# Kernel tuning notes

Measured on AMD Instinct MI355X. Metric: run time of the kernel, lower is better.

The kernel has to match this reference:

```python
import jax, jax.numpy as jnp
import numpy as np

B, K, IN, CH, M, N = 1024, 64, 128, 256, 4, 16


def setup_inputs() -> dict:
    key = jax.random.key(0)
    ks = jax.random.split(key, 12)
    s = 0.02
    return {
        "user_node": jax.random.normal(ks[0], (B, K, IN), jnp.float32),
        "RIS_node": jax.random.normal(ks[1], (B, IN), jnp.float32),
        "cas_channel": jax.random.normal(ks[2], (B, K, 2 * M * N), jnp.float32),
        "d_link": jax.random.normal(ks[3], (B, K, 2 * M), jnp.float32),
        # f2_user: Linear(3*IN -> CH), ReLU, Linear(CH -> CH)
        "W1": jax.random.normal(ks[4], (3 * IN, CH), jnp.float32) * s,
        "b1": jnp.zeros((CH,), jnp.float32),
        "W2": jax.random.normal(ks[5], (CH, CH), jnp.float32) * s,
        "b2": jnp.zeros((CH,), jnp.float32),
        # f3_RIS: Linear(2*IN -> CH), ReLU, Linear(CH -> CH)
        "W3": jax.random.normal(ks[6], (2 * IN, CH), jnp.float32) * s,
        "b3": jnp.zeros((CH,), jnp.float32),
        "W4": jax.random.normal(ks[7], (CH, CH), jnp.float32) * s,
        "b4": jnp.zeros((CH,), jnp.float32),
    }


def _leave_one_out_max(x):
    # x: (B, K, D). Exact leave-one-out max via prefix/suffix cummax, O(K).
    prefix = jax.lax.cummax(x, axis=1)                      # max over 0..k
    suffix = jax.lax.cummax(x[:, ::-1], axis=1)[:, ::-1]    # max over k..K-1
    neg = jnp.full_like(x[:, :1], -jnp.inf)
    left = jnp.concatenate([neg, prefix[:, :-1]], axis=1)   # max over 0..k-1
    right = jnp.concatenate([suffix[:, 1:], neg], axis=1)   # max over k+1..K-1
    return jnp.maximum(left, right)


def reference(user_node, RIS_node, cas_channel, d_link,
              W1, b1, W2, b2, W3, b3, W4, b4):
    b, k, d = user_node.shape
    mean_user = jnp.mean(user_node, axis=1)                 # (B, IN)
    loo_max = _leave_one_out_max(user_node)                 # (B, K, IN)
    ris_b = jnp.broadcast_to(RIS_node[:, None, :], (b, k, d))
    feat = jnp.concatenate([user_node, loo_max, ris_b], axis=-1)  # (B, K, 3*IN)
    h_user = jax.nn.relu(feat @ W1 + b1) @ W2 + b2          # (B, K, CH)
    user_node_update = jnp.concatenate([user_node, h_user], axis=-1)  # (B,K,IN+CH)
    rfeat = jnp.concatenate([RIS_node, mean_user], axis=-1)  # (B, 2*IN)
    h_ris = jax.nn.relu(rfeat @ W3 + b3) @ W4 + b4          # (B, CH)
    RIS_node_update = jnp.concatenate([RIS_node, h_ris], axis=-1)    # (B, IN+CH)
    return user_node_update, RIS_node_update
```

## Files before the change

kernel.cpp:

```cpp
#include <hip/hip_runtime.h>

typedef __attribute__((ext_vector_type(8))) short short8;
typedef __attribute__((ext_vector_type(4))) float f32x4;
typedef __attribute__((ext_vector_type(4))) int i32x4;

__device__ __forceinline__ unsigned short f2bf(float f) {
  unsigned u = __builtin_bit_cast(unsigned, f);
  u += 0x7fffu + ((u >> 16) & 1u);
  return (unsigned short)(u >> 16);
}

__global__ __launch_bounds__(256) void prep(
    const float* __restrict__ user, const float* __restrict__ ris,
    const float* __restrict__ W1, const float* __restrict__ W2,
    const float* __restrict__ W3, const float* __restrict__ W4,
    unsigned short* __restrict__ m1b, unsigned short* __restrict__ m2b,
    int* __restrict__ am, unsigned short* __restrict__ meanb,
    unsigned short* __restrict__ risb,
    unsigned short* __restrict__ W1f, unsigned short* __restrict__ W2f,
    unsigned short* __restrict__ W3f, unsigned short* __restrict__ W4f,
    float* __restrict__ out0, float* __restrict__ out1) {
  if (blockIdx.x < 512) {
    int idx = blockIdx.x * 256 + threadIdx.x;
    int b = idx >> 7, i = idx & 127;
    const float* up = user + (size_t)(b * 64) * 128 + i;
    float* op = out0 + (size_t)(b * 64) * 384 + i;
    float s = 0.f, m1 = -3.402823466e38f, m2 = -3.402823466e38f;
    int amx = 0;
    #pragma unroll 8
    for (int k = 0; k < 64; ++k) {
      float u = up[(size_t)k * 128];
      op[(size_t)k * 384] = u;
      s += u;
      if (u > m1) { m2 = m1; m1 = u; amx = k; }
      else if (u > m2) { m2 = u; }
    }
    m1b[idx] = f2bf(m1);
    m2b[idx] = f2bf(m2);
    am[idx] = amx;
    meanb[idx] = f2bf(s * (1.f / 64.f));
    float rv = ris[idx];
    out1[(size_t)b * 384 + i] = rv;
    risb[idx] = f2bf(rv);
  } else {
    int idx = (blockIdx.x - 512) * 256 + threadIdx.x;
    const float* src; unsigned short* dst; int kb; int rel;
    if (idx < 98304)        { src = W1; dst = W1f; kb = 12; rel = idx; }
    else if (idx < 163840)  { src = W2; dst = W2f; kb = 8;  rel = idx - 98304; }
    else if (idx < 229376)  { src = W3; dst = W3f; kb = 8;  rel = idx - 163840; }
    else                    { src = W4; dst = W4f; kb = 8;  rel = idx - 229376; }
    int kk = rel >> 8, n = rel & 255;
    int lane = (n & 15) | (((kk >> 3) & 3) << 4);
    int di = (((n >> 4) * kb + (kk >> 5)) * 64 + lane) * 8 + (kk & 7);
    dst[di] = f2bf(src[rel]);
  }
}

template<int MODE>
__device__ __forceinline__ void mlp_body(
    int bx, unsigned short* __restrict__ Hb,
    const float* __restrict__ user,
    const unsigned short* __restrict__ m1b, const unsigned short* __restrict__ m2b,
    const int* __restrict__ am,
    const unsigned short* __restrict__ risb, const unsigned short* __restrict__ meanb,
    const unsigned short* __restrict__ Wa, const unsigned short* __restrict__ Wb,
    const float* __restrict__ ba, const float* __restrict__ bb,
    float* __restrict__ out) {
  constexpr int NFS = (MODE == 0) ? 12 : 8;

  const int tid = threadIdx.x;
  const int lane = tid & 63, wn = tid >> 6;
  const int row0 = bx * 64;
  const int r = lane & 15;
  const int k8 = (lane >> 4) * 8;

  f32x4 acc[4][4];
  #pragma unroll
  for (int a = 0; a < 4; ++a)
    #pragma unroll
    for (int q = 0; q < 4; ++q) acc[a][q] = (f32x4)0.f;

  #pragma unroll
  for (int fs = 0; fs < NFS; ++fs) {
    short8 af[4];
    if constexpr (MODE == 0) {
      if (fs < 4) {
        #pragma unroll
        for (int mf = 0; mf < 4; ++mf) {
          const float* p = &user[(size_t)(row0 + mf * 16 + r) * 128 + fs * 32 + k8];
          f32x4 t0 = *(const f32x4*)p;
          f32x4 t1 = *(const f32x4*)(p + 4);
          short8 t;
          #pragma unroll
          for (int j = 0; j < 4; ++j) { t[j] = (short)f2bf(t0[j]); t[4 + j] = (short)f2bf(t1[j]); }
          af[mf] = t;
        }
      } else if (fs < 8) {
        int c0 = bx * 128 + (fs - 4) * 32 + k8;
        short8 m1v = *(const short8*)&m1b[c0];
        short8 m2v = *(const short8*)&m2b[c0];
        i32x4 a0 = *(const i32x4*)&am[c0];
        i32x4 a1 = *(const i32x4*)&am[c0 + 4];
        #pragma unroll
        for (int mf = 0; mf < 4; ++mf) {
          int rr = mf * 16 + r;
          short8 t;
          #pragma unroll
          for (int j = 0; j < 4; ++j) {
            t[j]     = (a0[j] == rr) ? m2v[j]     : m1v[j];
            t[4 + j] = (a1[j] == rr) ? m2v[4 + j] : m1v[4 + j];
          }
          af[mf] = t;
        }
      } else {
        short8 v = *(const short8*)&risb[bx * 128 + (fs - 8) * 32 + k8];
        #pragma unroll
        for (int mf = 0; mf < 4; ++mf) af[mf] = v;
      }
    } else {
      const unsigned short* src = (fs < 4) ? risb : meanb;
      #pragma unroll
      for (int mf = 0; mf < 4; ++mf)
        af[mf] = *(const short8*)&src[(size_t)(row0 + mf * 16 + r) * 128 + (fs & 3) * 32 + k8];
    }
    short8 bfr[4];
    #pragma unroll
    for (int nf = 0; nf < 4; ++nf)
      bfr[nf] = *(const short8*)&Wa[(size_t)(((wn * 4 + nf) * NFS + fs) * 64 + lane) * 8];
    #pragma unroll
    for (int mf = 0; mf < 4; ++mf)
      #pragma unroll
      for (int nf = 0; nf < 4; ++nf)
        acc[mf][nf] = __builtin_amdgcn_mfma_f32_16x16x32_bf16(af[mf], bfr[nf], acc[mf][nf], 0, 0, 0);
  }

  float bav[4];
  #pragma unroll
  for (int nf = 0; nf < 4; ++nf) bav[nf] = ba[wn * 64 + nf * 16 + (lane & 15)];
  #pragma unroll
  for (int mf = 0; mf < 4; ++mf)
    #pragma unroll
    for (int nf = 0; nf < 4; ++nf)
      #pragma unroll
      for (int j = 0; j < 4; ++j) {
        int rr = mf * 16 + ((lane >> 4) * 4) + j;
        int col = wn * 64 + nf * 16 + (lane & 15);
        int c = col >> 3;
        Hb[rr * 256 + ((c ^ (rr & 7)) << 3) + (col & 7)] =
            f2bf(fmaxf(acc[mf][nf][j] + bav[nf], 0.f));
      }
  __syncthreads();

  #pragma unroll
  for (int a = 0; a < 4; ++a)
    #pragma unroll
    for (int q = 0; q < 4; ++q) acc[a][q] = (f32x4)0.f;
  #pragma unroll
  for (int kc = 0; kc < 8; ++kc) {
    short8 af[4], bfr[4];
    #pragma unroll
    for (int mf = 0; mf < 4; ++mf) {
      int rr = mf * 16 + (lane & 15);
      int c = kc * 4 + (lane >> 4);
      af[mf] = *(const short8*)(Hb + rr * 256 + ((c ^ (rr & 7)) << 3));
    }
    #pragma unroll
    for (int nf = 0; nf < 4; ++nf)
      bfr[nf] = *(const short8*)&Wb[(size_t)(((wn * 4 + nf) * 8 + kc) * 64 + lane) * 8];
    #pragma unroll
    for (int mf = 0; mf < 4; ++mf)
      #pragma unroll
      for (int nf = 0; nf < 4; ++nf)
        acc[mf][nf] = __builtin_amdgcn_mfma_f32_16x16x32_bf16(af[mf], bfr[nf], acc[mf][nf], 0, 0, 0);
  }

  float bbv[4];
  #pragma unroll
  for (int nf = 0; nf < 4; ++nf) bbv[nf] = bb[wn * 64 + nf * 16 + (lane & 15)];
  #pragma unroll
  for (int mf = 0; mf < 4; ++mf)
    #pragma unroll
    for (int nf = 0; nf < 4; ++nf)
      #pragma unroll
      for (int j = 0; j < 4; ++j) {
        int rr = mf * 16 + ((lane >> 4) * 4) + j;
        int col = wn * 64 + nf * 16 + (lane & 15);
        out[(size_t)(row0 + rr) * 384 + 128 + col] = acc[mf][nf][j] + bbv[nf];
      }
}

__global__ __launch_bounds__(256, 4) void fused(
    const float* __restrict__ user,
    const unsigned short* __restrict__ m1b, const unsigned short* __restrict__ m2b,
    const int* __restrict__ am,
    const unsigned short* __restrict__ risb, const unsigned short* __restrict__ meanb,
    const unsigned short* __restrict__ W1f, const unsigned short* __restrict__ W2f,
    const unsigned short* __restrict__ W3f, const unsigned short* __restrict__ W4f,
    const float* __restrict__ b1, const float* __restrict__ b2,
    const float* __restrict__ b3, const float* __restrict__ b4,
    float* __restrict__ out0, float* __restrict__ out1) {
  __shared__ unsigned short Hb[64 * 256];
  if (blockIdx.x < 1024)
    mlp_body<0>(blockIdx.x, Hb, user, m1b, m2b, am, risb, meanb,
                W1f, W2f, b1, b2, out0);
  else
    mlp_body<1>(blockIdx.x - 1024, Hb, user, m1b, m2b, am, risb, meanb,
                W3f, W4f, b3, b4, out1);
}

extern "C" void kernel_launch(void* const* d_in, const int* in_sizes, int n_in,
                              void* d_out, int out_size, void* d_ws, size_t ws_size,
                              hipStream_t stream) {
  const float* user = (const float*)d_in[0];
  const float* ris  = (const float*)d_in[1];
  const float* W1 = (const float*)d_in[4];
  const float* b1 = (const float*)d_in[5];
  const float* W2 = (const float*)d_in[6];
  const float* b2 = (const float*)d_in[7];
  const float* W3 = (const float*)d_in[8];
  const float* b3 = (const float*)d_in[9];
  const float* W4 = (const float*)d_in[10];
  const float* b4 = (const float*)d_in[11];

  float* out0 = (float*)d_out;
  float* out1 = out0 + (size_t)65536 * 384;

  char* ws = (char*)d_ws;
  unsigned short* m1b   = (unsigned short*)(ws);
  unsigned short* m2b   = (unsigned short*)(ws + 262144);
  int*            amv   = (int*)(ws + 524288);
  unsigned short* meanb = (unsigned short*)(ws + 1048576);
  unsigned short* risb  = (unsigned short*)(ws + 1310720);
  unsigned short* W1f   = (unsigned short*)(ws + 1572864);
  unsigned short* W2f   = (unsigned short*)(ws + 1769472);
  unsigned short* W3f   = (unsigned short*)(ws + 1900544);
  unsigned short* W4f   = (unsigned short*)(ws + 2031616);

  hipLaunchKernelGGL(prep, dim3(1664), dim3(256), 0, stream,
                     user, ris, W1, W2, W3, W4,
                     m1b, m2b, amv, meanb, risb,
                     W1f, W2f, W3f, W4f, out0, out1);
  hipLaunchKernelGGL(fused, dim3(1040), dim3(256), 0, stream,
                     user, m1b, m2b, amv, risb, meanb,
                     W1f, W2f, W3f, W4f, b1, b2, b3, b4, out0, out1);
}
```

Before: 80.67 us.

## Split fused two-layer MLP into separate layer kernels with LDS-staged weight slices

Replaces the single fused MLP kernel with two kernels: the first computes the ReLU hidden layer per 64-column quarter, staging that weight slice in shared memory and writing bf16 hidden activations to a global workspace; the second reads them back and applies the second layer per column quarter. The aim is to let each block hold only a quarter of the weights in LDS for reuse across 256 rows and to raise occupancy. The cost is a 32MB round trip of intermediate activations through global memory, an extra launch, and first-layer A-fragments recomputed by four blocks. It falls back to the fused kernel if the workspace is too small.

```diff
diff --git a/kernel.cpp b/kernel.cpp
--- a/kernel.cpp
+++ b/kernel.cpp
@@ -56,6 +56,202 @@
   }
 }
 
+
+template<int MODE>
+__device__ __forceinline__ void l1_body(
+    int q, int rg, unsigned short* __restrict__ Wl,
+    const float* __restrict__ user,
+    const unsigned short* __restrict__ m1b, const unsigned short* __restrict__ m2b,
+    const int* __restrict__ am,
+    const unsigned short* __restrict__ risb, const unsigned short* __restrict__ meanb,
+    const unsigned short* __restrict__ Wsrc, const float* __restrict__ bsrc,
+    unsigned short* __restrict__ Hdst) {
+  constexpr int NFS = (MODE == 0) ? 12 : 8;
+  constexpr int NR  = (MODE == 0) ? 65536 : 1024;
+  const int tid = threadIdx.x;
+
+  #pragma unroll
+  for (int it = 0; it < NFS; ++it)
+    ((i32x4*)Wl)[it * 256 + tid] = ((const i32x4*)Wsrc)[it * 256 + tid];
+  __syncthreads();
+
+  const int lane = tid & 63, w = tid >> 6;
+  const int r = lane & 15;
+  const int k8 = (lane >> 4) * 8;
+  const int row0 = rg * 256 + w * 64;
+  const int b = row0 >> 6;
+
+  f32x4 acc[4][4];
+  #pragma unroll
+  for (int a = 0; a < 4; ++a)
+    #pragma unroll
+    for (int p = 0; p < 4; ++p) acc[a][p] = (f32x4)0.f;
+
+  #pragma unroll
+  for (int fs = 0; fs < NFS; ++fs) {
+    short8 af[4];
+    if constexpr (MODE == 0) {
+      if (fs < 4) {
+        #pragma unroll
+        for (int mf = 0; mf < 4; ++mf) {
+          const float* p = &user[(size_t)(row0 + mf * 16 + r) * 128 + fs * 32 + k8];
+          f32x4 t0 = *(const f32x4*)p;
+          f32x4 t1 = *(const f32x4*)(p + 4);
+          short8 t;
+          #pragma unroll
+          for (int j = 0; j < 4; ++j) { t[j] = (short)f2bf(t0[j]); t[4 + j] = (short)f2bf(t1[j]); }
+          af[mf] = t;
+        }
+      } else if (fs < 8) {
+        int c0 = b * 128 + (fs - 4) * 32 + k8;
+        short8 m1v = *(const short8*)&m1b[c0];
+        short8 m2v = *(const short8*)&m2b[c0];
+        i32x4 a0 = *(const i32x4*)&am[c0];
+        i32x4 a1 = *(const i32x4*)&am[c0 + 4];
+        #pragma unroll
+        for (int mf = 0; mf < 4; ++mf) {
+          int rr = mf * 16 + r;
+          short8 t;
+          #pragma unroll
+          for (int j = 0; j < 4; ++j) {
+            t[j]     = (a0[j] == rr) ? m2v[j]     : m1v[j];
+            t[4 + j] = (a1[j] == rr) ? m2v[4 + j] : m1v[4 + j];
+          }
+          af[mf] = t;
+        }
+      } else {
+        short8 v = *(const short8*)&risb[b * 128 + (fs - 8) * 32 + k8];
+        #pragma unroll
+        for (int mf = 0; mf < 4; ++mf) af[mf] = v;
+      }
+    } else {
+      const unsigned short* src = (fs < 4) ? risb : meanb;
+      #pragma unroll
+      for (int mf = 0; mf < 4; ++mf)
+        af[mf] = *(const short8*)&src[(size_t)(row0 + mf * 16 + r) * 128 + (fs & 3) * 32 + k8];
+    }
+    short8 bfr[4];
+    #pragma unroll
+    for (int nf = 0; nf < 4; ++nf)
+      bfr[nf] = *(const short8*)&Wl[((nf * NFS + fs) * 64 + lane) * 8];
+    #pragma unroll
+    for (int mf = 0; mf < 4; ++mf)
+      #pragma unroll
+      for (int nf = 0; nf < 4; ++nf)
+        acc[mf][nf] = __builtin_amdgcn_mfma_f32_16x16x32_bf16(af[mf], bfr[nf], acc[mf][nf], 0, 0, 0);
+  }
+
+  float bav[4];
+  #pragma unroll
+  for (int nf = 0; nf < 4; ++nf) bav[nf] = bsrc[q * 64 + nf * 16 + (lane & 15)];
+  #pragma unroll
+  for (int mf = 0; mf < 4; ++mf)
+    #pragma unroll
+    for (int nf = 0; nf < 4; ++nf)
+      #pragma unroll
+      for (int j = 0; j < 4; ++j) {
+        int row = row0 + mf * 16 + ((lane >> 4) * 4) + j;
+        int c = nf * 16 + (lane & 15);
+        Hdst[((size_t)q * NR + row) * 64 + c] = f2bf(fmaxf(acc[mf][nf][j] + bav[nf], 0.f));
+      }
+}
+
+__global__ __launch_bounds__(256, 3) void l1k(
+    const float* __restrict__ user,
+    const unsigned short* __restrict__ m1b, const unsigned short* __restrict__ m2b,
+    const int* __restrict__ am,
+    const unsigned short* __restrict__ risb, const unsigned short* __restrict__ meanb,
+    const unsigned short* __restrict__ W1f, const unsigned short* __restrict__ W3f,
+    const float* __restrict__ b1, const float* __restrict__ b3,
+    unsigned short* __restrict__ Hu, unsigned short* __restrict__ Hr) {
+  __shared__ unsigned short Wl[12 * 2048];
+  int bid = blockIdx.x;
+  if (bid < 1024) {
+    int q = bid & 3, rg = bid >> 2;
+    l1_body<0>(q, rg, Wl, user, m1b, m2b, am, risb, meanb,
+               W1f + (size_t)q * 4 * 12 * 512, b1, Hu);
+  } else {
+    int b2 = bid - 1024;
+    int q = b2 & 3, rg = b2 >> 2;
+    l1_body<1>(q, rg, Wl, user, m1b, m2b, am, risb, meanb,
+               W3f + (size_t)q * 4 * 8 * 512, b3, Hr);
+  }
+}
+
+template<int MODE>
+__device__ __forceinline__ void l2_body(
+    int q, int rg, unsigned short* __restrict__ Wl,
+    const unsigned short* __restrict__ H,
+    const unsigned short* __restrict__ Wsrc, const float* __restrict__ bsrc,
+    float* __restrict__ out) {
+  constexpr int NR = (MODE == 0) ? 65536 : 1024;
+  const int tid = threadIdx.x;
+
+  #pragma unroll
+  for (int it = 0; it < 8; ++it)
+    ((i32x4*)Wl)[it * 256 + tid] = ((const i32x4*)Wsrc)[it * 256 + tid];
+  __syncthreads();
+
+  const int lane = tid & 63, w = tid >> 6;
+  const int r = lane & 15;
+  const int k8 = (lane >> 4) * 8;
+  const int row0 = rg * 256 + w * 64;
+
+  f32x4 acc[4][4];
+  #pragma unroll
+  for (int a = 0; a < 4; ++a)
+    #pragma unroll
+    for (int p = 0; p < 4; ++p) acc[a][p] = (f32x4)0.f;
+
+  #pragma unroll
+  for (int kc = 0; kc < 8; ++kc) {
+    short8 af[4], bfr[4];
+    #pragma unroll
+    for (int mf = 0; mf < 4; ++mf)
+      af[mf] = *(const short8*)&H[((size_t)(kc >> 1) * NR + row0 + mf * 16 + r) * 64 +
+                                  (kc & 1) * 32 + k8];
+    #pragma unroll
+    for (int nf = 0; nf < 4; ++nf)
+      bfr[nf] = *(const short8*)&Wl[((nf * 8 + kc) * 64 + lane) * 8];
+    #pragma unroll
+    for (int mf = 0; mf < 4; ++mf)
+      #pragma unroll
+      for (int nf = 0; nf < 4; ++nf)
+        acc[mf][nf] = __builtin_amdgcn_mfma_f32_16x16x32_bf16(af[mf], bfr[nf], acc[mf][nf], 0, 0, 0);
+  }
+
+  float bbv[4];
+  #pragma unroll
+  for (int nf = 0; nf < 4; ++nf) bbv[nf] = bsrc[q * 64 + nf * 16 + (lane & 15)];
+  #pragma unroll
+  for (int mf = 0; mf < 4; ++mf)
+    #pragma unroll
+    for (int nf = 0; nf < 4; ++nf)
+      #pragma unroll
+      for (int j = 0; j < 4; ++j) {
+        int row = row0 + mf * 16 + ((lane >> 4) * 4) + j;
+        int c = nf * 16 + (lane & 15);
+        out[(size_t)row * 384 + 128 + q * 64 + c] = acc[mf][nf][j] + bbv[nf];
+      }
+}
+
+__global__ __launch_bounds__(256, 4) void l2k(
+    const unsigned short* __restrict__ Hu, const unsigned short* __restrict__ Hr,
+    const unsigned short* __restrict__ W2f, const unsigned short* __restrict__ W4f,
+    const float* __restrict__ b2, const float* __restrict__ b4,
+    float* __restrict__ out0, float* __restrict__ out1) {
+  __shared__ unsigned short Wl[8 * 2048];
+  int bid = blockIdx.x;
+  if (bid < 1024) {
+    int q = bid & 3, rg = bid >> 2;
+    l2_body<0>(q, rg, Wl, Hu, W2f + (size_t)q * 4 * 8 * 512, b2, out0);
+  } else {
+    int b2_ = bid - 1024;
+    int q = b2_ & 3, rg = b2_ >> 2;
+    l2_body<1>(q, rg, Wl, Hr, W4f + (size_t)q * 4 * 8 * 512, b4, out1);
+  }
+}
+
 template<int MODE>
 __device__ __forceinline__ void mlp_body(
     int bx, unsigned short* __restrict__ Hb,
@@ -67,7 +263,6 @@
     const float* __restrict__ ba, const float* __restrict__ bb,
     float* __restrict__ out) {
   constexpr int NFS = (MODE == 0) ? 12 : 8;
-
   const int tid = threadIdx.x;
   const int lane = tid & 63, wn = tid >> 6;
   const int row0 = bx * 64;
@@ -78,7 +273,7 @@
   #pragma unroll
   for (int a = 0; a < 4; ++a)
     #pragma unroll
-    for (int q = 0; q < 4; ++q) acc[a][q] = (f32x4)0.f;
+    for (int p = 0; p < 4; ++p) acc[a][p] = (f32x4)0.f;
 
   #pragma unroll
   for (int fs = 0; fs < NFS; ++fs) {
@@ -154,7 +349,7 @@
   #pragma unroll
   for (int a = 0; a < 4; ++a)
     #pragma unroll
-    for (int q = 0; q < 4; ++q) acc[a][q] = (f32x4)0.f;
+    for (int p = 0; p < 4; ++p) acc[a][p] = (f32x4)0.f;
   #pragma unroll
   for (int kc = 0; kc < 8; ++kc) {
     short8 af[4], bfr[4];
@@ -235,12 +430,23 @@
   unsigned short* W2f   = (unsigned short*)(ws + 1769472);
   unsigned short* W3f   = (unsigned short*)(ws + 1900544);
   unsigned short* W4f   = (unsigned short*)(ws + 2031616);
+  unsigned short* Hu    = (unsigned short*)(ws + 2162688);
+  unsigned short* Hr    = (unsigned short*)(ws + 2162688 + 33554432);
+  const size_t WS_NEED = 2162688 + 33554432 + 524288;
 
   hipLaunchKernelGGL(prep, dim3(1664), dim3(256), 0, stream,
                      user, ris, W1, W2, W3, W4,
                      m1b, m2b, amv, meanb, risb,
                      W1f, W2f, W3f, W4f, out0, out1);
-  hipLaunchKernelGGL(fused, dim3(1040), dim3(256), 0, stream,
-                     user, m1b, m2b, amv, risb, meanb,
-                     W1f, W2f, W3f, W4f, b1, b2, b3, b4, out0, out1);
-}
+  if (ws_size >= WS_NEED) {
+    hipLaunchKernelGGL(l1k, dim3(1040), dim3(256), 0, stream,
+                       user, m1b, m2b, amv, risb, meanb,
+                       W1f, W3f, b1, b3, Hu, Hr);
+    hipLaunchKernelGGL(l2k, dim3(1040), dim3(256), 0, stream,
+                       Hu, Hr, W2f, W4f, b2, b4, out0, out1);
+  } else {
+    hipLaunchKernelGGL(fused, dim3(1040), dim3(256), 0, stream,
+                       user, m1b, m2b, amv, risb, meanb,
+                       W1f, W2f, W3f, W4f, b1, b2, b3, b4, out0, out1);
+  }
+}
```

New measurement: 103.6 us. 1.28x slower.

## Pre-convert user features to bf16 and halve the row tile of fused MLP

Applied to the files above, without the earlier changes.

The prep kernel gains extra blocks that convert the whole user tensor to bf16 in workspace, so the fused kernel loads bf16 rows instead of converting fp32 on the fly. The fused MLP tile shrinks from 64 to 32 rows per block, doubling the grid and raising the occupancy hint to 8 blocks per CU, with the per-batch max and RIS lookups re-indexed to match. The aim is more blocks and less register and LDS pressure to hide latency. The cost is an extra full read of user plus a 16MB bf16 write, and twice as many weight-fragment loads per output row.

```diff
diff --git a/kernel.cpp b/kernel.cpp
--- a/kernel.cpp
+++ b/kernel.cpp
@@ -16,7 +16,7 @@
     const float* __restrict__ W3, const float* __restrict__ W4,
     unsigned short* __restrict__ m1b, unsigned short* __restrict__ m2b,
     int* __restrict__ am, unsigned short* __restrict__ meanb,
-    unsigned short* __restrict__ risb,
+    unsigned short* __restrict__ risb, unsigned short* __restrict__ userb,
     unsigned short* __restrict__ W1f, unsigned short* __restrict__ W2f,
     unsigned short* __restrict__ W3f, unsigned short* __restrict__ W4f,
     float* __restrict__ out0, float* __restrict__ out1) {
@@ -42,7 +42,7 @@
     float rv = ris[idx];
     out1[(size_t)b * 384 + i] = rv;
     risb[idx] = f2bf(rv);
-  } else {
+  } else if (blockIdx.x < 1664) {
     int idx = (blockIdx.x - 512) * 256 + threadIdx.x;
     const float* src; unsigned short* dst; int kb; int rel;
     if (idx < 98304)        { src = W1; dst = W1f; kb = 12; rel = idx; }
@@ -53,13 +53,21 @@
     int lane = (n & 15) | (((kk >> 3) & 3) << 4);
     int di = (((n >> 4) * kb + (kk >> 5)) * 64 + lane) * 8 + (kk & 7);
     dst[di] = f2bf(src[rel]);
+  } else {
+    size_t e = ((size_t)(blockIdx.x - 1664) * 256 + threadIdx.x) * 8;
+    f32x4 t0 = *(const f32x4*)(user + e);
+    f32x4 t1 = *(const f32x4*)(user + e + 4);
+    short8 t;
+    #pragma unroll
+    for (int j = 0; j < 4; ++j) { t[j] = (short)f2bf(t0[j]); t[4 + j] = (short)f2bf(t1[j]); }
+    *(short8*)(userb + e) = t;
   }
 }
 
 template<int MODE>
 __device__ __forceinline__ void mlp_body(
     int bx, unsigned short* __restrict__ Hb,
-    const float* __restrict__ user,
+    const unsigned short* __restrict__ userb,
     const unsigned short* __restrict__ m1b, const unsigned short* __restrict__ m2b,
     const int* __restrict__ am,
     const unsigned short* __restrict__ risb, const unsigned short* __restrict__ meanb,
@@ -67,43 +75,37 @@
     const float* __restrict__ ba, const float* __restrict__ bb,
     float* __restrict__ out) {
   constexpr int NFS = (MODE == 0) ? 12 : 8;
-
   const int tid = threadIdx.x;
   const int lane = tid & 63, wn = tid >> 6;
-  const int row0 = bx * 64;
+  const int row0 = bx * 32;
   const int r = lane & 15;
   const int k8 = (lane >> 4) * 8;
-
-  f32x4 acc[4][4];
-  #pragma unroll
-  for (int a = 0; a < 4; ++a)
-    #pragma unroll
-    for (int q = 0; q < 4; ++q) acc[a][q] = (f32x4)0.f;
+  const int b = row0 >> 6;
+  const int kbase = (bx & 1) * 32;
+
+  f32x4 acc[2][4];
+  #pragma unroll
+  for (int a = 0; a < 2; ++a)
+    #pragma unroll
+    for (int p = 0; p < 4; ++p) acc[a][p] = (f32x4)0.f;
 
   #pragma unroll
   for (int fs = 0; fs < NFS; ++fs) {
-    short8 af[4];
+    short8 af[2];
     if constexpr (MODE == 0) {
       if (fs < 4) {
         #pragma unroll
-        for (int mf = 0; mf < 4; ++mf) {
-          const float* p = &user[(size_t)(row0 + mf * 16 + r) * 128 + fs * 32 + k8];
-          f32x4 t0 = *(const f32x4*)p;
-          f32x4 t1 = *(const f32x4*)(p + 4);
-          short8 t;
-          #pragma unroll
-          for (int j = 0; j < 4; ++j) { t[j] = (short)f2bf(t0[j]); t[4 + j] = (short)f2bf(t1[j]); }
-          af[mf] = t;
-        }
+        for (int mf = 0; mf < 2; ++mf)
+          af[mf] = *(const short8*)&userb[(size_t)(row0 + mf * 16 + r) * 128 + fs * 32 + k8];
       } else if (fs < 8) {
-        int c0 = bx * 128 + (fs - 4) * 32 + k8;
+        int c0 = b * 128 + (fs - 4) * 32 + k8;
         short8 m1v = *(const short8*)&m1b[c0];
         short8 m2v = *(const short8*)&m2b[c0];
         i32x4 a0 = *(const i32x4*)&am[c0];
         i32x4 a1 = *(const i32x4*)&am[c0 + 4];
         #pragma unroll
-        for (int mf = 0; mf < 4; ++mf) {
-          int rr = mf * 16 + r;
+        for (int mf = 0; mf < 2; ++mf) {
+          int rr = kbase + mf * 16 + r;
           short8 t;
           #pragma unroll
           for (int j = 0; j < 4; ++j) {
@@ -113,14 +115,13 @@
           af[mf] = t;
         }
       } else {
-        short8 v = *(const short8*)&risb[bx * 128 + (fs - 8) * 32 + k8];
-        #pragma unroll
-        for (int mf = 0; mf < 4; ++mf) af[mf] = v;
+        short8 v = *(const short8*)&risb[b * 128 + (fs - 8) * 32 + k8];
+        af[0] = v; af[1] = v;
       }
     } else {
       const unsigned short* src = (fs < 4) ? risb : meanb;
       #pragma unroll
-      for (int mf = 0; mf < 4; ++mf)
+      for (int mf = 0; mf < 2; ++mf)
         af[mf] = *(const short8*)&src[(size_t)(row0 + mf * 16 + r) * 128 + (fs & 3) * 32 + k8];
     }
     short8 bfr[4];
@@ -128,7 +129,7 @@
     for (int nf = 0; nf < 4; ++nf)
       bfr[nf] = *(const short8*)&Wa[(size_t)(((wn * 4 + nf) * NFS + fs) * 64 + lane) * 8];
     #pragma unroll
-    for (int mf = 0; mf < 4; ++mf)
+    for (int mf = 0; mf < 2; ++mf)
       #pragma unroll
       for (int nf = 0; nf < 4; ++nf)
         acc[mf][nf] = __builtin_amdgcn_mfma_f32_16x16x32_bf16(af[mf], bfr[nf], acc[mf][nf], 0, 0, 0);
@@ -138,7 +139,7 @@
   #pragma unroll
   for (int nf = 0; nf < 4; ++nf) bav[nf] = ba[wn * 64 + nf * 16 + (lane & 15)];
   #pragma unroll
-  for (int mf = 0; mf < 4; ++mf)
+  for (int mf = 0; mf < 2; ++mf)
     #pragma unroll
     for (int nf = 0; nf < 4; ++nf)
       #pragma unroll
@@ -152,14 +153,14 @@
   __syncthreads();
 
   #pragma unroll
-  for (int a = 0; a < 4; ++a)
-    #pragma unroll
-    for (int q = 0; q < 4; ++q) acc[a][q] = (f32x4)0.f;
+  for (int a = 0; a < 2; ++a)
+    #pragma unroll
+    for (int p = 0; p < 4; ++p) acc[a][p] = (f32x4)0.f;
   #pragma unroll
   for (int kc = 0; kc < 8; ++kc) {
-    short8 af[4], bfr[4];
-    #pragma unroll
-    for (int mf = 0; mf < 4; ++mf) {
+    short8 af[2], bfr[4];
+    #pragma unroll
+    for (int mf = 0; mf < 2; ++mf) {
       int rr = mf * 16 + (lane & 15);
       int c = kc * 4 + (lane >> 4);
       af[mf] = *(const short8*)(Hb + rr * 256 + ((c ^ (rr & 7)) << 3));
@@ -168,7 +169,7 @@
     for (int nf = 0; nf < 4; ++nf)
       bfr[nf] = *(const short8*)&Wb[(size_t)(((wn * 4 + nf) * 8 + kc) * 64 + lane) * 8];
     #pragma unroll
-    for (int mf = 0; mf < 4; ++mf)
+    for (int mf = 0; mf < 2; ++mf)
       #pragma unroll
       for (int nf = 0; nf < 4; ++nf)
         acc[mf][nf] = __builtin_amdgcn_mfma_f32_16x16x32_bf16(af[mf], bfr[nf], acc[mf][nf], 0, 0, 0);
@@ -178,7 +179,7 @@
   #pragma unroll
   for (int nf = 0; nf < 4; ++nf) bbv[nf] = bb[wn * 64 + nf * 16 + (lane & 15)];
   #pragma unroll
-  for (int mf = 0; mf < 4; ++mf)
+  for (int mf = 0; mf < 2; ++mf)
     #pragma unroll
     for (int nf = 0; nf < 4; ++nf)
       #pragma unroll
@@ -189,8 +190,8 @@
       }
 }
 
-__global__ __launch_bounds__(256, 4) void fused(
-    const float* __restrict__ user,
+__global__ __launch_bounds__(256, 8) void fused(
+    const unsigned short* __restrict__ userb,
     const unsigned short* __restrict__ m1b, const unsigned short* __restrict__ m2b,
     const int* __restrict__ am,
     const unsigned short* __restrict__ risb, const unsigned short* __restrict__ meanb,
@@ -199,12 +200,12 @@
     const float* __restrict__ b1, const float* __restrict__ b2,
     const float* __restrict__ b3, const float* __restrict__ b4,
     float* __restrict__ out0, float* __restrict__ out1) {
-  __shared__ unsigned short Hb[64 * 256];
-  if (blockIdx.x < 1024)
-    mlp_body<0>(blockIdx.x, Hb, user, m1b, m2b, am, risb, meanb,
+  __shared__ unsigned short Hb[32 * 256];
+  if (blockIdx.x < 2048)
+    mlp_body<0>(blockIdx.x, Hb, userb, m1b, m2b, am, risb, meanb,
                 W1f, W2f, b1, b2, out0);
   else
-    mlp_body<1>(blockIdx.x - 1024, Hb, user, m1b, m2b, am, risb, meanb,
+    mlp_body<1>(blockIdx.x - 2048, Hb, userb, m1b, m2b, am, risb, meanb,
                 W3f, W4f, b3, b4, out1);
 }
 
@@ -235,12 +236,13 @@
   unsigned short* W2f   = (unsigned short*)(ws + 1769472);
   unsigned short* W3f   = (unsigned short*)(ws + 1900544);
   unsigned short* W4f   = (unsigned short*)(ws + 2031616);
-
-  hipLaunchKernelGGL(prep, dim3(1664), dim3(256), 0, stream,
+  unsigned short* userb = (unsigned short*)(ws + 2162688);
+
+  hipLaunchKernelGGL(prep, dim3(5760), dim3(256), 0, stream,
                      user, ris, W1, W2, W3, W4,
-                     m1b, m2b, amv, meanb, risb,
+                     m1b, m2b, amv, meanb, risb, userb,
                      W1f, W2f, W3f, W4f, out0, out1);
-  hipLaunchKernelGGL(fused, dim3(1040), dim3(256), 0, stream,
-                     user, m1b, m2b, amv, risb, meanb,
+  hipLaunchKernelGGL(fused, dim3(2080), dim3(256), 0, stream,
+                     userb, m1b, m2b, amv, risb, meanb,
                      W1f, W2f, W3f, W4f, b1, b2, b3, b4, out0, out1);
 }
```

Measured after the change: 181.9 us. +125.5%, slower.

## Make MLP kernel persistent with register-resident weights and pre-converted bf16 user input

Applied to the files above, without the earlier changes.

Replaces the per-tile fused kernel with a persistent kernel of 256 blocks × 512 threads. Each of the 8 waves keeps its 32-column slice of W1 and W2 in registers and loops over 4 batch tiles, so weights are no longer re-fetched for every tile. The prep kernel gains extra blocks that convert user_node to a bf16 workspace, halving the bytes the MLP reads for that operand. This adds an extra global write/read pass, makes register pressure high with 40 short8 weight fragments per thread, and gives lower occupancy and parallelism. The small RIS MLP runs on only 16 blocks at the tail of the kernel.

```diff
diff --git a/kernel.cpp b/kernel.cpp
--- a/kernel.cpp
+++ b/kernel.cpp
@@ -16,7 +16,7 @@
     const float* __restrict__ W3, const float* __restrict__ W4,
     unsigned short* __restrict__ m1b, unsigned short* __restrict__ m2b,
     int* __restrict__ am, unsigned short* __restrict__ meanb,
-    unsigned short* __restrict__ risb,
+    unsigned short* __restrict__ risb, unsigned short* __restrict__ userb,
     unsigned short* __restrict__ W1f, unsigned short* __restrict__ W2f,
     unsigned short* __restrict__ W3f, unsigned short* __restrict__ W4f,
     float* __restrict__ out0, float* __restrict__ out1) {
@@ -42,7 +42,7 @@
     float rv = ris[idx];
     out1[(size_t)b * 384 + i] = rv;
     risb[idx] = f2bf(rv);
-  } else {
+  } else if (blockIdx.x < 1664) {
     int idx = (blockIdx.x - 512) * 256 + threadIdx.x;
     const float* src; unsigned short* dst; int kb; int rel;
     if (idx < 98304)        { src = W1; dst = W1f; kb = 12; rel = idx; }
@@ -53,144 +53,19 @@
     int lane = (n & 15) | (((kk >> 3) & 3) << 4);
     int di = (((n >> 4) * kb + (kk >> 5)) * 64 + lane) * 8 + (kk & 7);
     dst[di] = f2bf(src[rel]);
+  } else {
+    size_t e = ((size_t)(blockIdx.x - 1664) * 256 + threadIdx.x) * 8;
+    f32x4 t0 = *(const f32x4*)(user + e);
+    f32x4 t1 = *(const f32x4*)(user + e + 4);
+    short8 t;
+    #pragma unroll
+    for (int j = 0; j < 4; ++j) { t[j] = (short)f2bf(t0[j]); t[4 + j] = (short)f2bf(t1[j]); }
+    *(short8*)(userb + e) = t;
   }
 }
 
-template<int MODE>
-__device__ __forceinline__ void mlp_body(
-    int bx, unsigned short* __restrict__ Hb,
-    const float* __restrict__ user,
-    const unsigned short* __restrict__ m1b, const unsigned short* __restrict__ m2b,
-    const int* __restrict__ am,
-    const unsigned short* __restrict__ risb, const unsigned short* __restrict__ meanb,
-    const unsigned short* __restrict__ Wa, const unsigned short* __restrict__ Wb,
-    const float* __restrict__ ba, const float* __restrict__ bb,
-    float* __restrict__ out) {
-  constexpr int NFS = (MODE == 0) ? 12 : 8;
-
-  const int tid = threadIdx.x;
-  const int lane = tid & 63, wn = tid >> 6;
-  const int row0 = bx * 64;
-  const int r = lane & 15;
-  const int k8 = (lane >> 4) * 8;
-
-  f32x4 acc[4][4];
-  #pragma unroll
-  for (int a = 0; a < 4; ++a)
-    #pragma unroll
-    for (int q = 0; q < 4; ++q) acc[a][q] = (f32x4)0.f;
-
-  #pragma unroll
-  for (int fs = 0; fs < NFS; ++fs) {
-    short8 af[4];
-    if constexpr (MODE == 0) {
-      if (fs < 4) {
-        #pragma unroll
-        for (int mf = 0; mf < 4; ++mf) {
-          const float* p = &user[(size_t)(row0 + mf * 16 + r) * 128 + fs * 32 + k8];
-          f32x4 t0 = *(const f32x4*)p;
-          f32x4 t1 = *(const f32x4*)(p + 4);
-          short8 t;
-          #pragma unroll
-          for (int j = 0; j < 4; ++j) { t[j] = (short)f2bf(t0[j]); t[4 + j] = (short)f2bf(t1[j]); }
-          af[mf] = t;
-        }
-      } else if (fs < 8) {
-        int c0 = bx * 128 + (fs - 4) * 32 + k8;
-        short8 m1v = *(const short8*)&m1b[c0];
-        short8 m2v = *(const short8*)&m2b[c0];
-        i32x4 a0 = *(const i32x4*)&am[c0];
-        i32x4 a1 = *(const i32x4*)&am[c0 + 4];
-        #pragma unroll
-        for (int mf = 0; mf < 4; ++mf) {
-          int rr = mf * 16 + r;
-          short8 t;
-          #pragma unroll
-          for (int j = 0; j < 4; ++j) {
-            t[j]     = (a0[j] == rr) ? m2v[j]     : m1v[j];
-            t[4 + j] = (a1[j] == rr) ? m2v[4 + j] : m1v[4 + j];
-          }
-          af[mf] = t;
-        }
-      } else {
-        short8 v = *(const short8*)&risb[bx * 128 + (fs - 8) * 32 + k8];
-        #pragma unroll
-        for (int mf = 0; mf < 4; ++mf) af[mf] = v;
-      }
-    } else {
-      const unsigned short* src = (fs < 4) ? risb : meanb;
-      #pragma unroll
-      for (int mf = 0; mf < 4; ++mf)
-        af[mf] = *(const short8*)&src[(size_t)(row0 + mf * 16 + r) * 128 + (fs & 3) * 32 + k8];
-    }
-    short8 bfr[4];
-    #pragma unroll
-    for (int nf = 0; nf < 4; ++nf)
-      bfr[nf] = *(const short8*)&Wa[(size_t)(((wn * 4 + nf) * NFS + fs) * 64 + lane) * 8];
-    #pragma unroll
-    for (int mf = 0; mf < 4; ++mf)
-      #pragma unroll
-      for (int nf = 0; nf < 4; ++nf)
-        acc[mf][nf] = __builtin_amdgcn_mfma_f32_16x16x32_bf16(af[mf], bfr[nf], acc[mf][nf], 0, 0, 0);
-  }
-
-  float bav[4];
-  #pragma unroll
-  for (int nf = 0; nf < 4; ++nf) bav[nf] = ba[wn * 64 + nf * 16 + (lane & 15)];
-  #pragma unroll
-  for (int mf = 0; mf < 4; ++mf)
-    #pragma unroll
-    for (int nf = 0; nf < 4; ++nf)
-      #pragma unroll
-      for (int j = 0; j < 4; ++j) {
-        int rr = mf * 16 + ((lane >> 4) * 4) + j;
-        int col = wn * 64 + nf * 16 + (lane & 15);
-        int c = col >> 3;
-        Hb[rr * 256 + ((c ^ (rr & 7)) << 3) + (col & 7)] =
-            f2bf(fmaxf(acc[mf][nf][j] + bav[nf], 0.f));
-      }
-  __syncthreads();
-
-  #pragma unroll
-  for (int a = 0; a < 4; ++a)
-    #pragma unroll
-    for (int q = 0; q < 4; ++q) acc[a][q] = (f32x4)0.f;
-  #pragma unroll
-  for (int kc = 0; kc < 8; ++kc) {
-    short8 af[4], bfr[4];
-    #pragma unroll
-    for (int mf = 0; mf < 4; ++mf) {
-      int rr = mf * 16 + (lane & 15);
-      int c = kc * 4 + (lane >> 4);
-      af[mf] = *(const short8*)(Hb + rr * 256 + ((c ^ (rr & 7)) << 3));
-    }
-    #pragma unroll
-    for (int nf = 0; nf < 4; ++nf)
-      bfr[nf] = *(const short8*)&Wb[(size_t)(((wn * 4 + nf) * 8 + kc) * 64 + lane) * 8];
-    #pragma unroll
-    for (int mf = 0; mf < 4; ++mf)
-      #pragma unroll
-      for (int nf = 0; nf < 4; ++nf)
-        acc[mf][nf] = __builtin_amdgcn_mfma_f32_16x16x32_bf16(af[mf], bfr[nf], acc[mf][nf], 0, 0, 0);
-  }
-
-  float bbv[4];
-  #pragma unroll
-  for (int nf = 0; nf < 4; ++nf) bbv[nf] = bb[wn * 64 + nf * 16 + (lane & 15)];
-  #pragma unroll
-  for (int mf = 0; mf < 4; ++mf)
-    #pragma unroll
-    for (int nf = 0; nf < 4; ++nf)
-      #pragma unroll
-      for (int j = 0; j < 4; ++j) {
-        int rr = mf * 16 + ((lane >> 4) * 4) + j;
-        int col = wn * 64 + nf * 16 + (lane & 15);
-        out[(size_t)(row0 + rr) * 384 + 128 + col] = acc[mf][nf][j] + bbv[nf];
-      }
-}
-
-__global__ __launch_bounds__(256, 4) void fused(
-    const float* __restrict__ user,
+__global__ __launch_bounds__(512, 2) void persist(
+    const unsigned short* __restrict__ userb,
     const unsigned short* __restrict__ m1b, const unsigned short* __restrict__ m2b,
     const int* __restrict__ am,
     const unsigned short* __restrict__ risb, const unsigned short* __restrict__ meanb,
@@ -200,12 +75,198 @@
     const float* __restrict__ b3, const float* __restrict__ b4,
     float* __restrict__ out0, float* __restrict__ out1) {
   __shared__ unsigned short Hb[64 * 256];
-  if (blockIdx.x < 1024)
-    mlp_body<0>(blockIdx.x, Hb, user, m1b, m2b, am, risb, meanb,
-                W1f, W2f, b1, b2, out0);
-  else
-    mlp_body<1>(blockIdx.x - 1024, Hb, user, m1b, m2b, am, risb, meanb,
-                W3f, W4f, b3, b4, out1);
+
+  const int tid = threadIdx.x;
+  const int lane = tid & 63, wn = tid >> 6;
+  const int r = lane & 15;
+  const int k8 = (lane >> 4) * 8;
+  const int j4 = (lane >> 4) * 4;
+
+  short8 wA[24], wB[16];
+  #pragma unroll
+  for (int nf = 0; nf < 2; ++nf)
+    #pragma unroll
+    for (int fs = 0; fs < 12; ++fs)
+      wA[nf * 12 + fs] = *(const short8*)&W1f[(size_t)(((wn * 2 + nf) * 12 + fs) * 64 + lane) * 8];
+  #pragma unroll
+  for (int nf = 0; nf < 2; ++nf)
+    #pragma unroll
+    for (int kc = 0; kc < 8; ++kc)
+      wB[nf * 8 + kc] = *(const short8*)&W2f[(size_t)(((wn * 2 + nf) * 8 + kc) * 64 + lane) * 8];
+
+  float ba[2] = { b1[wn * 32 + r], b1[wn * 32 + 16 + r] };
+  float bb[2] = { b2[wn * 32 + r], b2[wn * 32 + 16 + r] };
+
+  for (int it = 0; it < 4; ++it) {
+    const int b = blockIdx.x * 4 + it;
+    const int row0 = b * 64;
+
+    f32x4 acc[4][2];
+    #pragma unroll
+    for (int a = 0; a < 4; ++a) { acc[a][0] = (f32x4)0.f; acc[a][1] = (f32x4)0.f; }
+
+    #pragma unroll
+    for (int fs = 0; fs < 4; ++fs) {
+      short8 af[4];
+      #pragma unroll
+      for (int mf = 0; mf < 4; ++mf)
+        af[mf] = *(const short8*)&userb[(size_t)(row0 + mf * 16 + r) * 128 + fs * 32 + k8];
+      #pragma unroll
+      for (int mf = 0; mf < 4; ++mf)
+        #pragma unroll
+        for (int nf = 0; nf < 2; ++nf)
+          acc[mf][nf] = __builtin_amdgcn_mfma_f32_16x16x32_bf16(af[mf], wA[nf * 12 + fs], acc[mf][nf], 0, 0, 0);
+    }
+    #pragma unroll
+    for (int fs = 0; fs < 4; ++fs) {
+      int c0 = b * 128 + fs * 32 + k8;
+      short8 m1v = *(const short8*)&m1b[c0];
+      short8 m2v = *(const short8*)&m2b[c0];
+      i32x4 a0 = *(const i32x4*)&am[c0];
+      i32x4 a1 = *(const i32x4*)&am[c0 + 4];
+      #pragma unroll
+      for (int mf = 0; mf < 4; ++mf) {
+        int rr = mf * 16 + r;
+        short8 t;
+        #pragma unroll
+        for (int j = 0; j < 4; ++j) {
+          t[j]     = (a0[j] == rr) ? m2v[j]     : m1v[j];
+          t[4 + j] = (a1[j] == rr) ? m2v[4 + j] : m1v[4 + j];
+        }
+        #pragma unroll
+        for (int nf = 0; nf < 2; ++nf)
+          acc[mf][nf] = __builtin_amdgcn_mfma_f32_16x16x32_bf16(t, wA[nf * 12 + 4 + fs], acc[mf][nf], 0, 0, 0);
+      }
+    }
+    #pragma unroll
+    for (int fs = 0; fs < 4; ++fs) {
+      short8 v = *(const short8*)&risb[b * 128 + fs * 32 + k8];
+      #pragma unroll
+      for (int mf = 0; mf < 4; ++mf)
+        #pragma unroll
+        for (int nf = 0; nf < 2; ++nf)
+          acc[mf][nf] = __builtin_amdgcn_mfma_f32_16x16x32_bf16(v, wA[nf * 12 + 8 + fs], acc[mf][nf], 0, 0, 0);
+    }
+
+    #pragma unroll
+    for (int mf = 0; mf < 4; ++mf)
+      #pragma unroll
+      for (int nf = 0; nf < 2; ++nf)
+        #pragma unroll
+        for (int j = 0; j < 4; ++j) {
+          int rr = mf * 16 + j4 + j;
+          int col = wn * 32 + nf * 16 + r;
+          int c = col >> 3;
+          Hb[rr * 256 + ((c ^ (rr & 7)) << 3) + (col & 7)] =
+              f2bf(fmaxf(acc[mf][nf][j] + ba[nf], 0.f));
+        }
+    __syncthreads();
+
+    f32x4 acc2[4][2];
+    #pragma unroll
+    for (int a = 0; a < 4; ++a) { acc2[a][0] = (f32x4)0.f; acc2[a][1] = (f32x4)0.f; }
+    #pragma unroll
+    for (int kc = 0; kc < 8; ++kc) {
+      short8 af[4];
+      #pragma unroll
+      for (int mf = 0; mf < 4; ++mf) {
+        int rr = mf * 16 + r;
+        int c = kc * 4 + (lane >> 4);
+        af[mf] = *(const short8*)(Hb + rr * 256 + ((c ^ (rr & 7)) << 3));
+      }
+      #pragma unroll
+      for (int mf = 0; mf < 4; ++mf)
+        #pragma unroll
+        for (int nf = 0; nf < 2; ++nf)
+          acc2[mf][nf] = __builtin_amdgcn_mfma_f32_16x16x32_bf16(af[mf], wB[nf * 8 + kc], acc2[mf][nf], 0, 0, 0);
+    }
+
+    #pragma unroll
+    for (int mf = 0; mf < 4; ++mf)
+      #pragma unroll
+      for (int nf = 0; nf < 2; ++nf)
+        #pragma unroll
+        for (int j = 0; j < 4; ++j) {
+          int rr = mf * 16 + j4 + j;
+          int col = wn * 32 + nf * 16 + r;
+          out0[(size_t)(row0 + rr) * 384 + 128 + col] = acc2[mf][nf][j] + bb[nf];
+        }
+    __syncthreads();
+  }
+
+  if (blockIdx.x < 16) {
+    #pragma unroll
+    for (int nf = 0; nf < 2; ++nf)
+      #pragma unroll
+      for (int fs = 0; fs < 8; ++fs)
+        wA[nf * 12 + fs] = *(const short8*)&W3f[(size_t)(((wn * 2 + nf) * 8 + fs) * 64 + lane) * 8];
+    #pragma unroll
+    for (int nf = 0; nf < 2; ++nf)
+      #pragma unroll
+      for (int kc = 0; kc < 8; ++kc)
+        wB[nf * 8 + kc] = *(const short8*)&W4f[(size_t)(((wn * 2 + nf) * 8 + kc) * 64 + lane) * 8];
+    float ba3[2] = { b3[wn * 32 + r], b3[wn * 32 + 16 + r] };
+    float bb4[2] = { b4[wn * 32 + r], b4[wn * 32 + 16 + r] };
+    const int row0 = blockIdx.x * 64;
+
+    f32x4 acc[4][2];
+    #pragma unroll
+    for (int a = 0; a < 4; ++a) { acc[a][0] = (f32x4)0.f; acc[a][1] = (f32x4)0.f; }
+    #pragma unroll
+    for (int fs = 0; fs < 8; ++fs) {
+      const unsigned short* src = (fs < 4) ? risb : meanb;
+      short8 af[4];
+      #pragma unroll
+      for (int mf = 0; mf < 4; ++mf)
+        af[mf] = *(const short8*)&src[(size_t)(row0 + mf * 16 + r) * 128 + (fs & 3) * 32 + k8];
+      #pragma unroll
+      for (int mf = 0; mf < 4; ++mf)
+        #pragma unroll
+        for (int nf = 0; nf < 2; ++nf)
+          acc[mf][nf] = __builtin_amdgcn_mfma_f32_16x16x32_bf16(af[mf], wA[nf * 12 + fs], acc[mf][nf], 0, 0, 0);
+    }
+    #pragma unroll
+    for (int mf = 0; mf < 4; ++mf)
+      #pragma unroll
+      for (int nf = 0; nf < 2; ++nf)
+        #pragma unroll
+        for (int j = 0; j < 4; ++j) {
+          int rr = mf * 16 + j4 + j;
+          int col = wn * 32 + nf * 16 + r;
+          int c = col >> 3;
+          Hb[rr * 256 + ((c ^ (rr & 7)) << 3) + (col & 7)] =
+              f2bf(fmaxf(acc[mf][nf][j] + ba3[nf], 0.f));
+        }
+    __syncthreads();
+    f32x4 acc2[4][2];
+    #pragma unroll
+    for (int a = 0; a < 4; ++a) { acc2[a][0] = (f32x4)0.f; acc2[a][1] = (f32x4)0.f; }
+    #pragma unroll
+    for (int kc = 0; kc < 8; ++kc) {
+      short8 af[4];
+      #pragma unroll
+      for (int mf = 0; mf < 4; ++mf) {
+        int rr = mf * 16 + r;
+        int c = kc * 4 + (lane >> 4);
+        af[mf] = *(const short8*)(Hb + rr * 256 + ((c ^ (rr & 7)) << 3));
+      }
+      #pragma unroll
+      for (int mf = 0; mf < 4; ++mf)
+        #pragma unroll
+        for (int nf = 0; nf < 2; ++nf)
+          acc2[mf][nf] = __builtin_amdgcn_mfma_f32_16x16x32_bf16(af[mf], wB[nf * 8 + kc], acc2[mf][nf], 0, 0, 0);
+    }
+    #pragma unroll
+    for (int mf = 0; mf < 4; ++mf)
+      #pragma unroll
+      for (int nf = 0; nf < 2; ++nf)
+        #pragma unroll
+        for (int j = 0; j < 4; ++j) {
+          int rr = mf * 16 + j4 + j;
+          int col = wn * 32 + nf * 16 + r;
+          out1[(size_t)(row0 + rr) * 384 + 128 + col] = acc2[mf][nf][j] + bb4[nf];
+        }
+  }
 }
 
 extern "C" void kernel_launch(void* const* d_in, const int* in_sizes, int n_in,
@@ -235,12 +296,13 @@
   unsigned short* W2f   = (unsigned short*)(ws + 1769472);
   unsigned short* W3f   = (unsigned short*)(ws + 1900544);
   unsigned short* W4f   = (unsigned short*)(ws + 2031616);
-
-  hipLaunchKernelGGL(prep, dim3(1664), dim3(256), 0, stream,
+  unsigned short* userb = (unsigned short*)(ws + 2162688);
+
+  hipLaunchKernelGGL(prep, dim3(5760), dim3(256), 0, stream,
                      user, ris, W1, W2, W3, W4,
-                     m1b, m2b, amv, meanb, risb,
+                     m1b, m2b, amv, meanb, risb, userb,
                      W1f, W2f, W3f, W4f, out0, out1);
-  hipLaunchKernelGGL(fused, dim3(1040), dim3(256), 0, stream,
-                     user, m1b, m2b, amv, risb, meanb,
+  hipLaunchKernelGGL(persist, dim3(256), dim3(512), 0, stream,
+                     userb, m1b, m2b, amv, risb, meanb,
                      W1f, W2f, W3f, W4f, b1, b2, b3, b4, out0, out1);
 }
```

Measured after the change: 109.7 us. +36.0%, slower.
